# Optimization experiments

Hardware: AMD Instinct MI355X
Metric: run time of the kernel (lower is better)

## Reference

```python
import jax, jax.numpy as jnp
import numpy as np

HIDDEN = 2048
N_HEADS = 16
N_KV = 8
HEAD_DIM = 128
EPS = 1e-6
THETA = 1000000.0
T = 2048


def _rmsnorm(x, w):
    # x: [T, h, D]; normalize over last dim
    var = jnp.mean(x * x, axis=-1, keepdims=True)
    return x * jax.lax.rsqrt(var + EPS) * w


def _rope(x, positions):
    # neox-style rotate-half, rotary_dim == head_dim
    D = x.shape[-1]
    inv_freq = 1.0 / (THETA ** (jnp.arange(0, D, 2, dtype=jnp.float32) / D))  # [D/2]
    freqs = positions.astype(jnp.float32)[:, None] * inv_freq  # [T, D/2]
    cos = jnp.cos(freqs)[:, None, :]  # [T, 1, D/2]
    sin = jnp.sin(freqs)[:, None, :]
    x1, x2 = jnp.split(x, 2, axis=-1)
    return jnp.concatenate([x1 * cos - x2 * sin, x2 * cos + x1 * sin], axis=-1)


def setup_inputs() -> dict:
    key = jax.random.key(0)
    ks = jax.random.split(key, 7)
    s = 0.02
    return {
        "positions": jnp.arange(T, dtype=jnp.int32),
        "hidden_states": jax.random.normal(ks[0], (T, HIDDEN), dtype=jnp.float32),
        "wq": jax.random.normal(ks[1], (HIDDEN, N_HEADS * HEAD_DIM), dtype=jnp.float32) * s,
        "wk": jax.random.normal(ks[2], (HIDDEN, N_KV * HEAD_DIM), dtype=jnp.float32) * s,
        "wv": jax.random.normal(ks[3], (HIDDEN, N_KV * HEAD_DIM), dtype=jnp.float32) * s,
        "wo": jax.random.normal(ks[4], (N_HEADS * HEAD_DIM, HIDDEN), dtype=jnp.float32) * s,
        "q_norm_w": jnp.ones((HEAD_DIM,), dtype=jnp.float32),
        "k_norm_w": jnp.ones((HEAD_DIM,), dtype=jnp.float32),
    }


def reference(positions, hidden_states, wq, wk, wv, wo, q_norm_w, k_norm_w):
    q = (hidden_states @ wq).reshape(-1, N_HEADS, HEAD_DIM)
    k = (hidden_states @ wk).reshape(-1, N_KV, HEAD_DIM)
    v = (hidden_states @ wv).reshape(-1, N_KV, HEAD_DIM)
    q = _rmsnorm(q, q_norm_w)
    k = _rmsnorm(k, k_norm_w)
    q = _rope(q, positions)
    k = _rope(k, positions)
    # GQA: expand kv heads
    rep = N_HEADS // N_KV
    k = jnp.repeat(k, rep, axis=1)  # [T, H, D]
    v = jnp.repeat(v, rep, axis=1)
    scale = HEAD_DIM ** -0.5
    scores = jnp.einsum('qhd,khd->hqk', q, k) * scale  # [H, T, T]
    tq = q.shape[0]
    causal = jnp.tril(jnp.ones((tq, tq), dtype=bool))
    scores = jnp.where(causal[None], scores, jnp.finfo(scores.dtype).min)
    probs = jax.nn.softmax(scores, axis=-1)
    o = jnp.einsum('hqk,khd->qhd', probs, v).reshape(tq, N_HEADS * HEAD_DIM)
    return o @ wo
```

## Files before the change

### kernel.cpp

```cpp
#include <hip/hip_runtime.h>
#include <cstdint>

#define TT 2048
#define NH 16
#define NKV 8
#define HD 128
#define SCALE_L2E 0.12751743f
#define SM_M2 16.5f

typedef unsigned short u16;
typedef unsigned int u32;
typedef u16 u16x8 __attribute__((ext_vector_type(8)));
typedef __bf16 bf16x8 __attribute__((ext_vector_type(8)));
typedef float f32x4 __attribute__((ext_vector_type(4)));

__device__ inline u16 f2bf(float x){
  u32 u = __builtin_bit_cast(u32, x);
  u = (u + 0x7fffu + ((u >> 16) & 1u)) >> 16;
  return (u16)u;
}
__device__ inline float bf2f(u16 h){
  return __builtin_bit_cast(float, (u32)h << 16);
}
__device__ inline bf16x8 as_bf(u16x8 v){ return __builtin_bit_cast(bf16x8, v); }

__device__ inline void gl_lds16(const void* g, void* l){
  typedef __attribute__((address_space(1))) const void gv_t;
  typedef __attribute__((address_space(3))) void lv_t;
  __builtin_amdgcn_global_load_lds((gv_t*)g, (lv_t*)l, 16, 0, 0);
}

__global__ void cast_f32_bf16(const float* __restrict__ in, u16* __restrict__ out, int n8){
  int i = blockIdx.x * blockDim.x + threadIdx.x;
  if (i < n8){
    const float4* p = (const float4*)(in + (size_t)i * 8);
    float4 a = p[0], b = p[1];
    u16x8 o = { f2bf(a.x), f2bf(a.y), f2bf(a.z), f2bf(a.w),
                f2bf(b.x), f2bf(b.y), f2bf(b.z), f2bf(b.w) };
    *(u16x8*)(out + (size_t)i * 8) = o;
  }
}

__global__ void transpose_cast(const float* __restrict__ in, u16* __restrict__ out, int R, int C){
  __shared__ float tile[32][33];
  int bx = blockIdx.x * 32;
  int by = blockIdx.y * 32;
  int x = threadIdx.x, y = threadIdx.y;
  #pragma unroll
  for (int i = 0; i < 32; i += 8) tile[y + i][x] = in[(size_t)(by + y + i) * C + bx + x];
  __syncthreads();
  #pragma unroll
  for (int i = 0; i < 32; i += 8) out[(size_t)(bx + y + i) * R + by + x] = f2bf(tile[x][y + i]);
}

template<bool F32OUT>
__global__ __launch_bounds__(512, 2) void gemm8p(const u16* __restrict__ A, const u16* __restrict__ B,
                                                 void* __restrict__ Cv, int Klen,
                                                 int lda, int ldb, int ldc, size_t zstride){
  extern __shared__ u16 smem[];
  const int tid = threadIdx.x;
  const int wv = tid >> 6, ln = tid & 63;
  const int lg = ln >> 4, l15 = ln & 15;
  const int wr = wv >> 2, wc = wv & 3;
  const int m0 = blockIdx.y * 128, n0 = blockIdx.x * 256;
  const int Kofs = blockIdx.z * Klen;
  const u16* Ab0 = A + (size_t)m0 * lda + Kofs;
  const u16* Bb0 = B + (size_t)n0 * ldb + Kofs;
  f32x4 acc[4][4] = {};

  auto stage = [&](int sbuf, int kt){
    u16* base = smem + sbuf * 24576;
    const u16* Ak = Ab0 + kt * 64;
    #pragma unroll
    for (int it = 0; it < 2; ++it){
      int idx = it * 512 + tid;
      int r = idx >> 3, sl = idx & 7, g = sl ^ (r & 7);
      gl_lds16(Ak + (size_t)r * lda + g * 8, base + (it * 512 + wv * 64) * 8);
    }
    const u16* Bk = Bb0 + kt * 64;
    u16* bbase = base + 8192;
    #pragma unroll
    for (int it = 0; it < 4; ++it){
      int idx = it * 512 + tid;
      int r = idx >> 3, sl = idx & 7, g = sl ^ (r & 7);
      gl_lds16(Bk + (size_t)r * ldb + g * 8, bbase + (it * 512 + wv * 64) * 8);
    }
  };

  const int nk = Klen / 64;
  stage(0, 0);
  if (nk > 1) stage(1, 1);
  for (int kt = 0; kt < nk; ++kt){
    if (kt + 2 < nk){
      stage((kt + 2) % 3, kt + 2);
      asm volatile("s_waitcnt vmcnt(12)" ::: "memory");
    } else if (kt + 1 < nk){
      asm volatile("s_waitcnt vmcnt(6)" ::: "memory");
    } else {
      asm volatile("s_waitcnt vmcnt(0)" ::: "memory");
    }
    __builtin_amdgcn_s_barrier();
    const u16* lA = smem + (kt % 3) * 24576;
    const u16* lB = lA + 8192;
    #pragma unroll
    for (int kk = 0; kk < 2; ++kk){
      bf16x8 af[4], bfv[4];
      #pragma unroll
      for (int mm = 0; mm < 4; mm++){
        int ra = wr * 64 + mm * 16 + l15;
        int slot = (kk * 4 + lg) ^ (ra & 7);
        af[mm] = as_bf(*(const u16x8*)&lA[(ra * 8 + slot) * 8]);
      }
      #pragma unroll
      for (int nn = 0; nn < 4; nn++){
        int cb = wc * 64 + nn * 16 + l15;
        int slot = (kk * 4 + lg) ^ (cb & 7);
        bfv[nn] = as_bf(*(const u16x8*)&lB[(cb * 8 + slot) * 8]);
      }
      __builtin_amdgcn_s_setprio(1);
      #pragma unroll
      for (int mm = 0; mm < 4; mm++)
        #pragma unroll
        for (int nn = 0; nn < 4; nn++)
          acc[mm][nn] = __builtin_amdgcn_mfma_f32_16x16x32_bf16(af[mm], bfv[nn], acc[mm][nn], 0, 0, 0);
      __builtin_amdgcn_s_setprio(0);
      __builtin_amdgcn_s_barrier();
    }
  }
  #pragma unroll
  for (int mm = 0; mm < 4; mm++)
    #pragma unroll
    for (int nn = 0; nn < 4; nn++){
      int grow0 = m0 + wr * 64 + mm * 16 + lg * 4;
      int gcol  = n0 + wc * 64 + nn * 16 + l15;
      #pragma unroll
      for (int r = 0; r < 4; r++){
        float v = acc[mm][nn][r];
        if (F32OUT) ((float*)Cv + blockIdx.z * zstride)[(size_t)(grow0 + r) * ldc + gcol] = v;
        else        ((u16*)Cv)[(size_t)(grow0 + r) * ldc + gcol] = f2bf(v);
      }
    }
}

__global__ void add_f32(const float* __restrict__ a, const float* __restrict__ b,
                        float* __restrict__ o, int n4){
  int i = blockIdx.x * blockDim.x + threadIdx.x;
  if (i < n4){
    float4 x = ((const float4*)a)[i], y = ((const float4*)b)[i];
    float4 z = { x.x + y.x, x.y + y.y, x.z + y.z, x.w + y.w };
    ((float4*)o)[i] = z;
  }
}

__global__ void rmsnorm_rope(const u16* __restrict__ QKV, const int* __restrict__ pos,
                             const float* __restrict__ qw, const float* __restrict__ kw,
                             u16* __restrict__ Qr, u16* __restrict__ Kr){
  int gw = (blockIdx.x * blockDim.x + threadIdx.x) >> 6;
  int ln = threadIdx.x & 63;
  int t = gw / 24, idx = gw % 24;
  if (t >= TT) return;
  bool isq = idx < NH;
  int head = isq ? idx : idx - NH;
  const u16* src = QKV + (size_t)t * 4096 + (isq ? head * HD : 2048 + head * HD);
  const float* wgt = isq ? qw : kw;
  float x0 = bf2f(src[ln]), x1 = bf2f(src[ln + 64]);
  float ss = x0 * x0 + x1 * x1;
  #pragma unroll
  for (int off = 32; off; off >>= 1) ss += __shfl_xor(ss, off);
  float r = rsqrtf(ss * (1.0f / 128.0f) + 1e-6f);
  float xn0 = x0 * r * wgt[ln], xn1 = x1 * r * wgt[ln + 64];
  float inv = exp2f(-(float)ln * 0.311430758895690f);
  float ang = (float)pos[t] * inv;
  float c = cosf(ang), s = sinf(ang);
  float o0 = xn0 * c - xn1 * s;
  float o1 = xn1 * c + xn0 * s;
  u16* dst = isq ? (Qr + (size_t)t * 2048 + head * HD) : (Kr + (size_t)t * 1024 + head * HD);
  dst[ln]      = f2bf(o0);
  dst[ln + 64] = f2bf(o1);
}

__global__ void v_transpose(const u16* __restrict__ QKV, u16* __restrict__ Vt){
  __shared__ u16 tile[64][72];
  int kh = blockIdx.z;
  int d0 = blockIdx.y * 64;
  int t0 = blockIdx.x * 64;
  int tid = threadIdx.x;
  #pragma unroll
  for (int it = 0; it < 2; ++it){
    int idx = it * 256 + tid;
    int tr = idx >> 3, seg = idx & 7;
    *(u16x8*)&tile[tr][seg * 8] =
      *(const u16x8*)(QKV + (size_t)(t0 + tr) * 4096 + 3072 + kh * HD + d0 + seg * 8);
  }
  __syncthreads();
  #pragma unroll
  for (int it = 0; it < 2; ++it){
    int idx = it * 256 + tid;
    int dr = idx >> 3, seg = idx & 7;
    u16x8 v;
    #pragma unroll
    for (int j = 0; j < 8; j++) v[j] = tile[seg * 8 + j][dr];
    *(u16x8*)(Vt + ((size_t)kh * HD + d0 + dr) * 2048 + t0 + seg * 8) = v;
  }
}

__global__ __launch_bounds__(512, 4) void attn(const u16* __restrict__ Qr, const u16* __restrict__ Kr,
                                               const u16* __restrict__ Vt, u16* __restrict__ O){
  extern __shared__ u16 smem[];
  u16* Karea = smem;
  u16* Varea = smem + 16384;
  const int h = blockIdx.y, kh = h >> 1;
  const int qc = (h < 8) ? blockIdx.x : 31 - blockIdx.x;
  const int tid = threadIdx.x, wv = tid >> 6, ln = tid & 63;
  const int i4 = wv & 3, jp = wv >> 2;
  const int lg = ln >> 4, l15 = ln & 15;
  u16* Pw = smem + 32768 + wv * 640;

  auto stage = [&](int buf, int it){
    const int tokl = tid >> 4;
    const int kp = tid & 15;
    const int seg = kp ^ (tokl & 7);
    #pragma unroll
    for (int p = 0; p < 2; ++p){
      int tokg = it * 64 + p * 32 + tokl;
      gl_lds16(Kr + (size_t)tokg * 1024 + kh * HD + seg * 8,
               Karea + (buf * 2 + p) * 4096 + wv * 512);
    }
    const u16* Vb = Vt + (size_t)kh * HD * 2048;
    const int dr = tid >> 2, slot = tid & 3;
    const int tokoff = (slot ^ (dr & 3)) * 8;
    #pragma unroll
    for (int p = 0; p < 2; ++p){
      gl_lds16(Vb + (size_t)dr * 2048 + it * 64 + p * 32 + tokoff,
               Varea + (buf * 2 + p) * 4096 + wv * 512);
    }
  };

  bf16x8 qf[4];
  {
    const u16* qp = Qr + (size_t)(qc * 64 + i4 * 16 + l15) * 2048 + h * HD + lg * 8;
    #pragma unroll
    for (int kk = 0; kk < 4; kk++) qf[kk] = as_bf(*(const u16x8*)(qp + kk * 32));
  }
  const u16x8 ones_u = {0x3f80, 0x3f80, 0x3f80, 0x3f80, 0x3f80, 0x3f80, 0x3f80, 0x3f80};
  const bf16x8 onesf = as_bf(ones_u);

  f32x4 acc[8] = {};
  f32x4 asum = {};

  stage(0, 0);
  const int nit = qc + 1;
  for (int it = 0; it < nit; ++it){
    const int buf = it & 1;
    __syncthreads();
    if (it + 1 < nit) stage(buf ^ 1, it + 1);
    const int t = 2 * it + jp;
    const int D0 = 32 * t - 64 * qc - 16 * i4;
    if (D0 <= 15){
      const u16* Kb = Karea + (buf * 2 + jp) * 4096;
      const u16* Vb2 = Varea + (buf * 2 + jp) * 4096;
      __builtin_amdgcn_s_setprio(1);
      f32x4 c0 = {}, c1 = {};
      if (D0 <= 0){
        #pragma unroll
        for (int kk = 0; kk < 4; ++kk){
          int slot = (kk * 4 + lg) ^ (l15 & 7);
          bf16x8 kf = as_bf(*(const u16x8*)&Kb[l15 * 128 + slot * 8]);
          c0 = __builtin_amdgcn_mfma_f32_16x16x32_bf16(qf[kk], kf, c0, 0, 0, 0);
        }
      }
      if (D0 + 16 <= 0){
        #pragma unroll
        for (int kk = 0; kk < 4; ++kk){
          int tok = 16 + l15;
          int slot = (kk * 4 + lg) ^ (tok & 7);
          bf16x8 kf = as_bf(*(const u16x8*)&Kb[tok * 128 + slot * 8]);
          c1 = __builtin_amdgcn_mfma_f32_16x16x32_bf16(qf[kk], kf, c1, 0, 0, 0);
        }
      }
      __builtin_amdgcn_s_setprio(0);
      #pragma unroll
      for (int s = 0; s < 2; ++s){
        const int D = D0 + 16 * s;
        #pragma unroll
        for (int r = 0; r < 4; ++r){
          int row = lg * 4 + r;
          float pv;
          if (D > 0) pv = 0.f;
          else {
            float x = (s ? c1[r] : c0[r]) * SCALE_L2E - SM_M2;
            if (D == 0 && l15 > row) x = -1e30f;
            pv = exp2f(x);
          }
          Pw[row * 40 + s * 16 + l15] = f2bf(pv);
        }
      }
      bf16x8 pf = as_bf(*(const u16x8*)&Pw[l15 * 40 + lg * 8]);
      __builtin_amdgcn_s_setprio(1);
      asum = __builtin_amdgcn_mfma_f32_16x16x32_bf16(pf, onesf, asum, 0, 0, 0);
      const int vslot = lg ^ (l15 & 3);
      #pragma unroll
      for (int g = 0; g < 8; ++g){
        int d = g * 16 + l15;
        bf16x8 vf = as_bf(*(const u16x8*)&Vb2[d * 32 + vslot * 8]);
        acc[g] = __builtin_amdgcn_mfma_f32_16x16x32_bf16(pf, vf, acc[g], 0, 0, 0);
      }
      __builtin_amdgcn_s_setprio(0);
    }
  }
  __syncthreads();
  float* Ls  = (float*)smem;
  float* LsS = (float*)smem + 8192;
  if (jp == 1){
    #pragma unroll
    for (int g = 0; g < 8; ++g)
      *(f32x4*)&Ls[i4 * 2048 + g * 256 + ln * 4] = acc[g];
    if (l15 == 0){
      #pragma unroll
      for (int r = 0; r < 4; ++r) LsS[i4 * 16 + lg * 4 + r] = asum[r];
    }
  }
  __syncthreads();
  if (jp == 0){
    float rinv[4];
    #pragma unroll
    for (int r = 0; r < 4; ++r)
      rinv[r] = 1.0f / (asum[r] + LsS[i4 * 16 + lg * 4 + r]);
    #pragma unroll
    for (int g = 0; g < 8; ++g){
      f32x4 po = *(const f32x4*)&Ls[i4 * 2048 + g * 256 + ln * 4];
      #pragma unroll
      for (int r = 0; r < 4; ++r){
        float o = (acc[g][r] + po[r]) * rinv[r];
        O[(size_t)(qc * 64 + i4 * 16 + lg * 4 + r) * 2048 + h * HD + g * 16 + l15] = f2bf(o);
      }
    }
  }
}

extern "C" void kernel_launch(void* const* d_in, const int* in_sizes, int n_in,
                              void* d_out, int out_size, void* d_ws, size_t ws_size,
                              hipStream_t stream){
  const int*   positions = (const int*)d_in[0];
  const float* hidden    = (const float*)d_in[1];
  const float* wq        = (const float*)d_in[2];
  const float* wk        = (const float*)d_in[3];
  const float* wv        = (const float*)d_in[4];
  const float* wo        = (const float*)d_in[5];
  const float* qw        = (const float*)d_in[6];
  const float* kw        = (const float*)d_in[7];
  float* out = (float*)d_out;

  char* ws = (char*)d_ws;
  u16* hs   = (u16*)ws; ws += (size_t)2048 * 2048 * 2;
  u16* Wqkv = (u16*)ws; ws += (size_t)4096 * 2048 * 2;
  u16* Wo   = (u16*)ws; ws += (size_t)2048 * 2048 * 2;
  u16* QKV  = (u16*)ws; ws += (size_t)2048 * 4096 * 2;
  u16* Qr   = (u16*)ws; ws += (size_t)2048 * 2048 * 2;
  u16* Kr   = (u16*)ws; ws += (size_t)2048 * 1024 * 2;
  u16* Vt   = (u16*)ws; ws += (size_t)8 * 128 * 2048 * 2;
  u16* O    = (u16*)ws;

  cast_f32_bf16<<<2048, 256, 0, stream>>>(hidden, hs, 2048 * 2048 / 8);
  dim3 tb(32, 8);
  transpose_cast<<<dim3(2048 / 32, 2048 / 32), tb, 0, stream>>>(wq, Wqkv, 2048, 2048);
  transpose_cast<<<dim3(1024 / 32, 2048 / 32), tb, 0, stream>>>(wk, Wqkv + (size_t)2048 * 2048, 2048, 1024);
  transpose_cast<<<dim3(1024 / 32, 2048 / 32), tb, 0, stream>>>(wv, Wqkv + (size_t)3072 * 2048, 2048, 1024);
  transpose_cast<<<dim3(2048 / 32, 2048 / 32), tb, 0, stream>>>(wo, Wo, 2048, 2048);

  gemm8p<false><<<dim3(16, 16, 1), 512, 147456, stream>>>(hs, Wqkv, QKV, 2048, 2048, 2048, 4096, 0);

  rmsnorm_rope<<<2048 * 24 / 4, 256, 0, stream>>>(QKV, positions, qw, kw, Qr, Kr);
  v_transpose<<<dim3(32, 2, 8), 256, 0, stream>>>(QKV, Vt);

  attn<<<dim3(32, 16), 512, 75776, stream>>>(Qr, Kr, Vt, O);

  float* p0 = (float*)QKV;
  gemm8p<true><<<dim3(8, 16, 2), 512, 147456, stream>>>(O, Wo, p0, 1024, 2048, 2048, 2048,
                                                        (size_t)2048 * 2048);
  add_f32<<<4096, 256, 0, stream>>>(p0, p0 + (size_t)2048 * 2048, out, 2048 * 2048 / 4);
}
```

Before: 159.9 us.

## Software-pipeline GEMM LDS fragment loads, swizzle block order, pack P writes in attention

```diff
diff --git a/kernel.cpp b/kernel.cpp
--- a/kernel.cpp
+++ b/kernel.cpp
@@ -62,70 +62,86 @@
   const int wv = tid >> 6, ln = tid & 63;
   const int lg = ln >> 4, l15 = ln & 15;
   const int wr = wv >> 2, wc = wv & 3;
-  const int m0 = blockIdx.y * 128, n0 = blockIdx.x * 256;
+  const int nbx = gridDim.x;
+  const int orig = blockIdx.x + nbx * blockIdx.y;
+  const int cpx = (nbx * gridDim.y) >> 3;
+  const int swz = (orig & 7) * cpx + (orig >> 3);
+  const int m0 = (swz / nbx) * 128, n0 = (swz % nbx) * 256;
   const int Kofs = blockIdx.z * Klen;
   const u16* Ab0 = A + (size_t)m0 * lda + Kofs;
   const u16* Bb0 = B + (size_t)n0 * ldb + Kofs;
   f32x4 acc[4][4] = {};
 
-  auto stage = [&](int sbuf, int kt){
+  auto stage = [&](int sbuf, int kt, int part){
     u16* base = smem + sbuf * 24576;
-    const u16* Ak = Ab0 + kt * 64;
-    #pragma unroll
-    for (int it = 0; it < 2; ++it){
-      int idx = it * 512 + tid;
-      int r = idx >> 3, sl = idx & 7, g = sl ^ (r & 7);
-      gl_lds16(Ak + (size_t)r * lda + g * 8, base + (it * 512 + wv * 64) * 8);
-    }
-    const u16* Bk = Bb0 + kt * 64;
-    u16* bbase = base + 8192;
-    #pragma unroll
-    for (int it = 0; it < 4; ++it){
-      int idx = it * 512 + tid;
-      int r = idx >> 3, sl = idx & 7, g = sl ^ (r & 7);
-      gl_lds16(Bk + (size_t)r * ldb + g * 8, bbase + (it * 512 + wv * 64) * 8);
+    if (part == 0){
+      const u16* Ak = Ab0 + kt * 64;
+      #pragma unroll
+      for (int it = 0; it < 2; ++it){
+        int idx = it * 512 + tid;
+        int r = idx >> 3, sl = idx & 7, g = sl ^ (r & 7);
+        gl_lds16(Ak + (size_t)r * lda + g * 8, base + (it * 512 + wv * 64) * 8);
+      }
+      const u16* Bk = Bb0 + kt * 64;
+      { int idx = tid; int r = idx >> 3, sl = idx & 7, g = sl ^ (r & 7);
+        gl_lds16(Bk + (size_t)r * ldb + g * 8, base + (8192 + wv * 64 * 8)); }
+    } else {
+      const u16* Bk = Bb0 + kt * 64;
+      #pragma unroll
+      for (int it = 1; it < 4; ++it){
+        int idx = it * 512 + tid;
+        int r = idx >> 3, sl = idx & 7, g = sl ^ (r & 7);
+        gl_lds16(Bk + (size_t)r * ldb + g * 8, base + (8192 + (it * 512 + wv * 64) * 8));
+      }
     }
   };
 
+  bf16x8 a0[4], b0[4], a1[4], b1[4];
+  auto ldfrags = [&](const u16* lA, bf16x8* af, bf16x8* bf, int kk){
+    const u16* lB = lA + 8192;
+    #pragma unroll
+    for (int mm = 0; mm < 4; mm++){
+      int ra = wr * 64 + mm * 16 + l15;
+      int sl = (kk * 4 + lg) ^ (ra & 7);
+      af[mm] = as_bf(*(const u16x8*)&lA[(ra * 8 + sl) * 8]);
+    }
+    #pragma unroll
+    for (int nn = 0; nn < 4; nn++){
+      int cb = wc * 64 + nn * 16 + l15;
+      int sl = (kk * 4 + lg) ^ (cb & 7);
+      bf[nn] = as_bf(*(const u16x8*)&lB[(cb * 8 + sl) * 8]);
+    }
+  };
+  auto mfma16 = [&](bf16x8* af, bf16x8* bf){
+    __builtin_amdgcn_s_setprio(1);
+    #pragma unroll
+    for (int mm = 0; mm < 4; mm++)
+      #pragma unroll
+      for (int nn = 0; nn < 4; nn++)
+        acc[mm][nn] = __builtin_amdgcn_mfma_f32_16x16x32_bf16(af[mm], bf[nn], acc[mm][nn], 0, 0, 0);
+    __builtin_amdgcn_s_setprio(0);
+  };
+
   const int nk = Klen / 64;
-  stage(0, 0);
-  if (nk > 1) stage(1, 1);
+  stage(0, 0, 0); stage(0, 0, 1);
+  stage(1, 1, 0); stage(1, 1, 1);
+  asm volatile("s_waitcnt vmcnt(6)" ::: "memory");
+  asm volatile("s_barrier" ::: "memory");
+  ldfrags(smem, a0, b0, 0);
+
   for (int kt = 0; kt < nk; ++kt){
-    if (kt + 2 < nk){
-      stage((kt + 2) % 3, kt + 2);
-      asm volatile("s_waitcnt vmcnt(12)" ::: "memory");
-    } else if (kt + 1 < nk){
-      asm volatile("s_waitcnt vmcnt(6)" ::: "memory");
-    } else {
-      asm volatile("s_waitcnt vmcnt(0)" ::: "memory");
-    }
-    __builtin_amdgcn_s_barrier();
     const u16* lA = smem + (kt % 3) * 24576;
-    const u16* lB = lA + 8192;
-    #pragma unroll
-    for (int kk = 0; kk < 2; ++kk){
-      bf16x8 af[4], bfv[4];
-      #pragma unroll
-      for (int mm = 0; mm < 4; mm++){
-        int ra = wr * 64 + mm * 16 + l15;
-        int slot = (kk * 4 + lg) ^ (ra & 7);
-        af[mm] = as_bf(*(const u16x8*)&lA[(ra * 8 + slot) * 8]);
-      }
-      #pragma unroll
-      for (int nn = 0; nn < 4; nn++){
-        int cb = wc * 64 + nn * 16 + l15;
-        int slot = (kk * 4 + lg) ^ (cb & 7);
-        bfv[nn] = as_bf(*(const u16x8*)&lB[(cb * 8 + slot) * 8]);
-      }
-      __builtin_amdgcn_s_setprio(1);
-      #pragma unroll
-      for (int mm = 0; mm < 4; mm++)
-        #pragma unroll
-        for (int nn = 0; nn < 4; nn++)
-          acc[mm][nn] = __builtin_amdgcn_mfma_f32_16x16x32_bf16(af[mm], bfv[nn], acc[mm][nn], 0, 0, 0);
-      __builtin_amdgcn_s_setprio(0);
-      __builtin_amdgcn_s_barrier();
-    }
+    ldfrags(lA, a1, b1, 1);
+    if (kt + 2 < nk) stage((kt + 2) % 3, kt + 2, 0);
+    mfma16(a0, b0);
+    if (kt + 2 < nk)      asm volatile("s_waitcnt vmcnt(3)" ::: "memory");
+    else if (kt + 1 < nk) asm volatile("s_waitcnt vmcnt(0)" ::: "memory");
+    asm volatile("s_barrier" ::: "memory");
+    if (kt + 1 < nk)
+      ldfrags(smem + ((kt + 1) % 3) * 24576, a0, b0, 0);
+    if (kt + 2 < nk) stage((kt + 2) % 3, kt + 2, 1);
+    mfma16(a1, b1);
+    asm volatile("s_barrier" ::: "memory");
   }
   #pragma unroll
   for (int mm = 0; mm < 4; mm++)
@@ -199,7 +215,11 @@
     int dr = idx >> 3, seg = idx & 7;
     u16x8 v;
     #pragma unroll
-    for (int j = 0; j < 8; j++) v[j] = tile[seg * 8 + j][dr];
+    for (int j = 0; j < 8; j++){
+      int p = seg * 8 + j;
+      int tsrc = (p & 32) | (((p & 31) >> 1) + 16 * (p & 1));
+      v[j] = tile[tsrc][dr];
+    }
     *(u16x8*)(Vt + ((size_t)kh * HD + d0 + dr) * 2048 + t0 + seg * 8) = v;
   }
 }
@@ -280,20 +300,23 @@
       }
       __builtin_amdgcn_s_setprio(0);
       #pragma unroll
-      for (int s = 0; s < 2; ++s){
-        const int D = D0 + 16 * s;
-        #pragma unroll
-        for (int r = 0; r < 4; ++r){
-          int row = lg * 4 + r;
-          float pv;
-          if (D > 0) pv = 0.f;
-          else {
-            float x = (s ? c1[r] : c0[r]) * SCALE_L2E - SM_M2;
-            if (D == 0 && l15 > row) x = -1e30f;
-            pv = exp2f(x);
-          }
-          Pw[row * 40 + s * 16 + l15] = f2bf(pv);
+      for (int r = 0; r < 4; ++r){
+        int row = lg * 4 + r;
+        float p0, p1;
+        if (D0 > 0) p0 = 0.f;
+        else {
+          float x = c0[r] * SCALE_L2E - SM_M2;
+          if (D0 == 0 && l15 > row) x = -1e30f;
+          p0 = exp2f(x);
         }
+        if (D0 + 16 > 0) p1 = 0.f;
+        else {
+          float x = c1[r] * SCALE_L2E - SM_M2;
+          if (D0 + 16 == 0 && l15 > row) x = -1e30f;
+          p1 = exp2f(x);
+        }
+        u32 pk = (__builtin_bit_cast(u32, p0) >> 16) | (__builtin_bit_cast(u32, p1) & 0xffff0000u);
+        *(u32*)&Pw[row * 40 + l15 * 2] = pk;
       }
       bf16x8 pf = as_bf(*(const u16x8*)&Pw[l15 * 40 + lg * 8]);
       __builtin_amdgcn_s_setprio(1);
```

Result: faster. 155.2 us (-2.9%).
